# Kernel optimization log

Measured on AMD Instinct MI355X. Metric: run time of the kernel, lower is better.

## Reference

```python
import jax, jax.numpy as jnp
import numpy as np

N = 50000
E = 800000
NEG_SLOPE = 0.2  # PyG GATConv default negative_slope


def _gat_layer(x, src, dst, W, a_src, a_dst, b, concat):
    # x: [N, Fin]; src/dst: [Etot] (self-loops already appended)
    H, O = a_src.shape
    n = x.shape[0]
    h = (x @ W).reshape(n, H, O)                      # [N, H, O]
    e_src = jnp.einsum('nho,ho->nh', h, a_src)        # [N, H]
    e_dst = jnp.einsum('nho,ho->nh', h, a_dst)
    alpha = e_src[src] + e_dst[dst]                   # [Etot, H]
    alpha = jnp.where(alpha >= 0, alpha, NEG_SLOPE * alpha)
    # segment softmax over destination nodes
    amax = jax.ops.segment_max(alpha, dst, num_segments=n)
    ex = jnp.exp(alpha - amax[dst])
    denom = jax.ops.segment_sum(ex, dst, num_segments=n)
    att = ex / (denom[dst] + 1e-16)                   # [Etot, H]
    msg = h[src] * att[:, :, None]                    # [Etot, H, O]
    agg = jax.ops.segment_sum(msg, dst, num_segments=n)  # [N, H, O]
    out = agg.reshape(n, H * O) if concat else agg.mean(axis=1)
    return out + b


def setup_inputs() -> dict:
    key = jax.random.key(0)
    k0, k1 = jax.random.split(key)
    inp = {
        'x': jax.random.normal(k0, (N, 2), jnp.float32),
        'edge_index': jax.random.randint(k1, (2, E), 0, N),
    }
    s = 0.1
    dims = [(2, 4, 64), (256, 4, 64), (256, 1, 2)]
    for i, (fin, H, O) in enumerate(dims):
        kw, ks, kd = jax.random.split(jax.random.fold_in(key, i + 10), 3)
        inp[f'W{i}'] = jax.random.normal(kw, (fin, H * O), jnp.float32) * s
        inp[f'a_src{i}'] = jax.random.normal(ks, (H, O), jnp.float32) * s
        inp[f'a_dst{i}'] = jax.random.normal(kd, (H, O), jnp.float32) * s
        inp[f'b{i}'] = jnp.zeros((H * O if i < 2 else O,), jnp.float32)
    return inp


def reference(x, edge_index, W0, a_src0, a_dst0, b0, W1, a_src1, a_dst1, b1,
              W2, a_src2, a_dst2, b2):
    n = x.shape[0]
    loops = jnp.arange(n, dtype=edge_index.dtype)  # PyG add_self_loops=True
    src = jnp.concatenate([edge_index[0], loops])
    dst = jnp.concatenate([edge_index[1], loops])
    h = jax.nn.relu(_gat_layer(x, src, dst, W0, a_src0, a_dst0, b0, True))
    h = jax.nn.relu(_gat_layer(h, src, dst, W1, a_src1, a_dst1, b1, True))
    h = jax.nn.relu(_gat_layer(h, src, dst, W2, a_src2, a_dst2, b2, False))
    return h
```

## Files before the change

### kernel.cpp

```cpp
#include <hip/hip_runtime.h>
#include <math.h>


typedef __attribute__((ext_vector_type(8))) short s16x8;
typedef __attribute__((ext_vector_type(4))) float f32x4;
typedef unsigned short u16;

__device__ __forceinline__ float wred_sum(float v){
  #pragma unroll
  for (int m = 32; m > 0; m >>= 1) v += __shfl_xor(v, m, 64);
  return v;
}
__device__ __forceinline__ void wred_sum4(float4& v){
  #pragma unroll
  for (int m = 32; m > 0; m >>= 1){
    v.x += __shfl_xor(v.x, m, 64);
    v.y += __shfl_xor(v.y, m, 64);
    v.z += __shfl_xor(v.z, m, 64);
    v.w += __shfl_xor(v.w, m, 64);
  }
}
__device__ __forceinline__ u16 bf16_rne(float x){
  unsigned int u = __float_as_uint(x);
  unsigned int r = u + 0x7FFFu + ((u >> 16) & 1u);
  return (u16)(r >> 16);
}

__global__ __launch_bounds__(256) void k_setup(const float* __restrict__ W1, u16* __restrict__ WhT,
                                               u16* __restrict__ WlT,
                                               const float* __restrict__ W0, const float* __restrict__ as0,
                                               const float* __restrict__ ad0, float* __restrict__ vs,
                                               int* __restrict__ deg, int N, int nblk_deg){
  int b = blockIdx.x;
  if (b < nblk_deg){
    int i = b * 256 + threadIdx.x;
    if (i < N) deg[i] = 1;
  } else if (b < nblk_deg + 256){
    int k = b - nblk_deg, j = threadIdx.x;
    float w = W1[k * 256 + j];
    u16 h = bf16_rne(w);
    float hf = __uint_as_float(((unsigned int)h) << 16);
    WhT[j * 256 + k] = h;
    WlT[j * 256 + k] = bf16_rne(w - hf);
  } else {
    int t = threadIdx.x;
    if (t < 8){
      int j = t >> 2, h = t & 3;
      float ss = 0.f, dd = 0.f;
      #pragma unroll 8
      for (int o = 0; o < 64; o++){
        float w = W0[j * 256 + h * 64 + o];
        ss = fmaf(w, as0[h * 64 + o], ss);
        dd = fmaf(w, ad0[h * 64 + o], dd);
      }
      vs[j * 4 + h]     = ss;
      vs[8 + j * 4 + h] = dd;
    }
  }
}

__global__ __launch_bounds__(256) void k_hist(const int* __restrict__ dst, int E, int* deg){
  int e = blockIdx.x * 256 + threadIdx.x;
  if (e < E) atomicAdd(&deg[dst[e]], 1);
}

__global__ __launch_bounds__(256) void k_scan_local(const int* __restrict__ deg, int* __restrict__ rowptr,
                                                    int* __restrict__ bsum, int N){
  __shared__ int sb[256];
  int t = threadIdx.x;
  int base = blockIdx.x * 2048 + t * 8;
  int d[8], s = 0;
  #pragma unroll
  for (int k = 0; k < 8; k++){
    d[k] = (base + k < N) ? deg[base + k] : 0;
    s += d[k];
  }
  sb[t] = s;
  __syncthreads();
  for (int off = 1; off < 256; off <<= 1){
    int v = (t >= off) ? sb[t - off] : 0;
    __syncthreads();
    sb[t] += v;
    __syncthreads();
  }
  int run = (t == 0) ? 0 : sb[t - 1];
  #pragma unroll
  for (int k = 0; k < 8; k++){
    if (base + k < N) rowptr[base + k] = run;
    run += d[k];
  }
  if (t == 255) bsum[blockIdx.x] = sb[255];
}

__global__ __launch_bounds__(64) void k_boff(const int* __restrict__ bsum, int* __restrict__ boff, int nb){
  __shared__ int sb[64];
  int t = threadIdx.x;
  int v = (t < nb) ? bsum[t] : 0;
  sb[t] = v;
  __syncthreads();
  for (int off = 1; off < 64; off <<= 1){
    int u = (t >= off) ? sb[t - off] : 0;
    __syncthreads();
    sb[t] += u;
    __syncthreads();
  }
  boff[t] = (t == 0) ? 0 : sb[t - 1];
  if (t == nb - 1) boff[nb] = sb[nb - 1];
}

__global__ __launch_bounds__(256) void k_finish(int* __restrict__ rowptr, const int* __restrict__ boff,
                                                int* __restrict__ ssrc, int* __restrict__ cursor,
                                                int N, int nb){
  int i = blockIdx.x * 256 + threadIdx.x;
  if (i < N){
    int p = rowptr[i] + boff[i >> 11];
    rowptr[i] = p;
    ssrc[p] = i;
    cursor[i] = p + 1;
  }
  if (i == 0) rowptr[N] = boff[nb];
}

__global__ __launch_bounds__(256) void k_scatter(const int* __restrict__ src, const int* __restrict__ dst,
                                                 int E, int* cursor, int* ssrc){
  int e = blockIdx.x * 256 + threadIdx.x;
  if (e < E){ int p = atomicAdd(&cursor[dst[e]], 1); ssrc[p] = src[e]; }
}

__global__ __launch_bounds__(256) void k_edge0(const float* __restrict__ X, const float* __restrict__ vs,
                                               const float* __restrict__ W0, const float* __restrict__ b0,
                                               const int* __restrict__ rowptr, const int* __restrict__ ssrc,
                                               float* __restrict__ X1, int N){
  int lane = threadIdx.x & 63;
  int n = blockIdx.x * 4 + (threadIdx.x >> 6);
  if (n >= N) return;
  int start = rowptr[n], deg = rowptr[n + 1] - start;
  float4 va = ((const float4*)vs)[0], vb = ((const float4*)vs)[1];
  float4 vc = ((const float4*)vs)[2], vd = ((const float4*)vs)[3];
  float2 xn = ((const float2*)X)[n];
  float4 ed4;
  ed4.x = fmaf(xn.x, vc.x, xn.y * vd.x); ed4.y = fmaf(xn.x, vc.y, xn.y * vd.y);
  ed4.z = fmaf(xn.x, vc.z, xn.y * vd.z); ed4.w = fmaf(xn.x, vc.w, xn.y * vd.w);

  float4 den = make_float4(0.f,0.f,0.f,0.f);
  float4 a0  = make_float4(0.f,0.f,0.f,0.f);
  float4 a1  = make_float4(0.f,0.f,0.f,0.f);
  for (int i = lane; i < deg; i += 64){
    int s = ssrc[start + i];
    float2 xs = ((const float2*)X)[s];
    float4 e;
    e.x = fmaf(xs.x, va.x, fmaf(xs.y, vb.x, ed4.x));
    e.y = fmaf(xs.x, va.y, fmaf(xs.y, vb.y, ed4.y));
    e.z = fmaf(xs.x, va.z, fmaf(xs.y, vb.z, ed4.z));
    e.w = fmaf(xs.x, va.w, fmaf(xs.y, vb.w, ed4.w));
    e.x = fmaxf(e.x, 0.2f*e.x); e.y = fmaxf(e.y, 0.2f*e.y);
    e.z = fmaxf(e.z, 0.2f*e.z); e.w = fmaxf(e.w, 0.2f*e.w);
    float4 wt;
    wt.x = __expf(e.x); wt.y = __expf(e.y);
    wt.z = __expf(e.z); wt.w = __expf(e.w);
    den.x += wt.x; den.y += wt.y; den.z += wt.z; den.w += wt.w;
    a0.x = fmaf(wt.x, xs.x, a0.x); a0.y = fmaf(wt.y, xs.x, a0.y);
    a0.z = fmaf(wt.z, xs.x, a0.z); a0.w = fmaf(wt.w, xs.x, a0.w);
    a1.x = fmaf(wt.x, xs.y, a1.x); a1.y = fmaf(wt.y, xs.y, a1.y);
    a1.z = fmaf(wt.z, xs.y, a1.z); a1.w = fmaf(wt.w, xs.y, a1.w);
  }
  wred_sum4(den); wred_sum4(a0); wred_sum4(a1);

  int hh = lane >> 4;
  float invd = 1.f / (((hh==0)?den.x:(hh==1)?den.y:(hh==2)?den.z:den.w) + 1e-16f);
  float g0 = ((hh==0)?a0.x:(hh==1)?a0.y:(hh==2)?a0.z:a0.w) * invd;
  float g1 = ((hh==0)?a1.x:(hh==1)?a1.y:(hh==2)?a1.z:a1.w) * invd;
  float4 w0r = ((const float4*)W0)[lane];
  float4 w1r = ((const float4*)(W0 + 256))[lane];
  float4 bb  = ((const float4*)b0)[lane];
  float4 v;
  v.x = fmaxf(fmaf(g0, w0r.x, fmaf(g1, w1r.x, bb.x)), 0.f);
  v.y = fmaxf(fmaf(g0, w0r.y, fmaf(g1, w1r.y, bb.y)), 0.f);
  v.z = fmaxf(fmaf(g0, w0r.z, fmaf(g1, w1r.z, bb.z)), 0.f);
  v.w = fmaxf(fmaf(g0, w0r.w, fmaf(g1, w1r.w, bb.w)), 0.f);
  ((float4*)(X1 + (size_t)n * 256))[lane] = v;
}

__global__ __launch_bounds__(256) void k_l1_mfma(const float* __restrict__ X,
                                                 const u16* __restrict__ WhT, const u16* __restrict__ WlT,
                                                 const float* __restrict__ as_, const float* __restrict__ ad_,
                                                 u16* __restrict__ Hh16, float* __restrict__ ES,
                                                 float* __restrict__ ED, int N){
  __shared__ u16 Ah[64 * 32], Al[64 * 32];
  __shared__ u16 Bh[256 * 32], Bl[256 * 32];
  int t = threadIdx.x;
  int wv = t >> 6, lane = t & 63;
  int lr = lane & 15, lg = lane >> 4;
  int rb = blockIdx.x * 64;

  f32x4 acc[16];
  #pragma unroll
  for (int c = 0; c < 16; c++) acc[c] = (f32x4){0.f, 0.f, 0.f, 0.f};

  int arow = t >> 2, aseg = t & 3;
  int agrow = rb + arow;

  for (int ks = 0; ks < 8; ks++){
    int k0 = ks * 32;
    __syncthreads();
    {
      float xv[8];
      if (agrow < N){
        const float4* p = (const float4*)(X + (size_t)agrow * 256 + k0 + aseg * 8);
        float4 v0 = p[0], v1 = p[1];
        xv[0]=v0.x; xv[1]=v0.y; xv[2]=v0.z; xv[3]=v0.w;
        xv[4]=v1.x; xv[5]=v1.y; xv[6]=v1.z; xv[7]=v1.w;
      } else {
        #pragma unroll
        for (int i = 0; i < 8; i++) xv[i] = 0.f;
      }
      union { u16 us[8]; uint4 v; } ph, pl;
      #pragma unroll
      for (int i = 0; i < 8; i++){
        u16 h = bf16_rne(xv[i]);
        float hf = __uint_as_float(((unsigned int)h) << 16);
        ph.us[i] = h;
        pl.us[i] = bf16_rne(xv[i] - hf);
      }
      *(uint4*)&Ah[arow * 32 + aseg * 8] = ph.v;
      *(uint4*)&Al[arow * 32 + aseg * 8] = pl.v;
    }
    #pragma unroll
    for (int i = 0; i < 4; i++){
      int chunk = i * 256 + t;
      int j = chunk >> 2, seg = chunk & 3;
      *(uint4*)&Bh[j * 32 + seg * 8] = *(const uint4*)&WhT[j * 256 + k0 + seg * 8];
      *(uint4*)&Bl[j * 32 + seg * 8] = *(const uint4*)&WlT[j * 256 + k0 + seg * 8];
    }
    __syncthreads();
    s16x8 ah = *(const s16x8*)&Ah[(wv * 16 + lr) * 32 + lg * 8];
    s16x8 al = *(const s16x8*)&Al[(wv * 16 + lr) * 32 + lg * 8];
    #pragma unroll
    for (int c = 0; c < 16; c++){
      s16x8 bh = *(const s16x8*)&Bh[(c * 16 + lr) * 32 + lg * 8];
      s16x8 bl = *(const s16x8*)&Bl[(c * 16 + lr) * 32 + lg * 8];
      acc[c] = __builtin_amdgcn_mfma_f32_16x16x32_bf16(ah, bh, acc[c], 0, 0, 0);
      acc[c] = __builtin_amdgcn_mfma_f32_16x16x32_bf16(ah, bl, acc[c], 0, 0, 0);
      acc[c] = __builtin_amdgcn_mfma_f32_16x16x32_bf16(al, bh, acc[c], 0, 0, 0);
    }
  }

  #pragma unroll
  for (int q = 0; q < 4; q++){
    int n = rb + wv * 16 + lg * 4 + q;
    if (n < N){
      union { _Float16 h[16]; uint4 v[2]; } pk;
      #pragma unroll
      for (int c = 0; c < 16; c++) pk.h[c] = (_Float16)acc[c][q];
      uint4* dstp = (uint4*)(Hh16 + (size_t)n * 256 + lr * 16);
      dstp[0] = pk.v[0];
      dstp[1] = pk.v[1];
    }
  }
  float es_p[4][4], ed_p[4][4];
  #pragma unroll
  for (int h = 0; h < 4; h++)
    #pragma unroll
    for (int q = 0; q < 4; q++){ es_p[h][q] = 0.f; ed_p[h][q] = 0.f; }
  #pragma unroll
  for (int c = 0; c < 16; c++){
    float asv = as_[c * 16 + lr];
    float adv = ad_[c * 16 + lr];
    int h = c >> 2;
    #pragma unroll
    for (int q = 0; q < 4; q++){
      es_p[h][q] = fmaf(acc[c][q], asv, es_p[h][q]);
      ed_p[h][q] = fmaf(acc[c][q], adv, ed_p[h][q]);
    }
  }
  #pragma unroll
  for (int h = 0; h < 4; h++)
    #pragma unroll
    for (int q = 0; q < 4; q++){
      #pragma unroll
      for (int mk = 1; mk < 16; mk <<= 1){
        es_p[h][q] += __shfl_xor(es_p[h][q], mk, 64);
        ed_p[h][q] += __shfl_xor(ed_p[h][q], mk, 64);
      }
    }
  if (lr == 0){
    #pragma unroll
    for (int q = 0; q < 4; q++){
      int n = rb + wv * 16 + lg * 4 + q;
      if (n < N){
        #pragma unroll
        for (int h = 0; h < 4; h++){
          ES[n * 4 + h] = es_p[h][q];
          ED[n * 4 + h] = ed_p[h][q];
        }
      }
    }
  }
}

__device__ __forceinline__ void agg_rows16(const u16* __restrict__ Hh, const int* ssh, const float* wrow,
                                           int cl, int lane, float* acc){
  union Cv { uint2 u; _Float16 h[4]; };
  int j = 0;
  for (; j + 7 < cl; j += 8){
    Cv r0, r1, r2, r3, r4, r5, r6, r7;
    float w0=wrow[j],w1=wrow[j+1],w2=wrow[j+2],w3=wrow[j+3];
    float w4=wrow[j+4],w5=wrow[j+5],w6=wrow[j+6],w7=wrow[j+7];
    r0.u = *(const uint2*)(Hh + (size_t)ssh[j  ] * 256 + 4*lane);
    r1.u = *(const uint2*)(Hh + (size_t)ssh[j+1] * 256 + 4*lane);
    r2.u = *(const uint2*)(Hh + (size_t)ssh[j+2] * 256 + 4*lane);
    r3.u = *(const uint2*)(Hh + (size_t)ssh[j+3] * 256 + 4*lane);
    r4.u = *(const uint2*)(Hh + (size_t)ssh[j+4] * 256 + 4*lane);
    r5.u = *(const uint2*)(Hh + (size_t)ssh[j+5] * 256 + 4*lane);
    r6.u = *(const uint2*)(Hh + (size_t)ssh[j+6] * 256 + 4*lane);
    r7.u = *(const uint2*)(Hh + (size_t)ssh[j+7] * 256 + 4*lane);
    #pragma unroll
    for (int k = 0; k < 4; k++) acc[k] = fmaf(w0, (float)r0.h[k], acc[k]);
    #pragma unroll
    for (int k = 0; k < 4; k++) acc[k] = fmaf(w1, (float)r1.h[k], acc[k]);
    #pragma unroll
    for (int k = 0; k < 4; k++) acc[k] = fmaf(w2, (float)r2.h[k], acc[k]);
    #pragma unroll
    for (int k = 0; k < 4; k++) acc[k] = fmaf(w3, (float)r3.h[k], acc[k]);
    #pragma unroll
    for (int k = 0; k < 4; k++) acc[k] = fmaf(w4, (float)r4.h[k], acc[k]);
    #pragma unroll
    for (int k = 0; k < 4; k++) acc[k] = fmaf(w5, (float)r5.h[k], acc[k]);
    #pragma unroll
    for (int k = 0; k < 4; k++) acc[k] = fmaf(w6, (float)r6.h[k], acc[k]);
    #pragma unroll
    for (int k = 0; k < 4; k++) acc[k] = fmaf(w7, (float)r7.h[k], acc[k]);
  }
  for (; j + 3 < cl; j += 4){
    Cv r0, r1, r2, r3;
    float w0=wrow[j],w1=wrow[j+1],w2=wrow[j+2],w3=wrow[j+3];
    r0.u = *(const uint2*)(Hh + (size_t)ssh[j  ] * 256 + 4*lane);
    r1.u = *(const uint2*)(Hh + (size_t)ssh[j+1] * 256 + 4*lane);
    r2.u = *(const uint2*)(Hh + (size_t)ssh[j+2] * 256 + 4*lane);
    r3.u = *(const uint2*)(Hh + (size_t)ssh[j+3] * 256 + 4*lane);
    #pragma unroll
    for (int k = 0; k < 4; k++) acc[k] = fmaf(w0, (float)r0.h[k], acc[k]);
    #pragma unroll
    for (int k = 0; k < 4; k++) acc[k] = fmaf(w1, (float)r1.h[k], acc[k]);
    #pragma unroll
    for (int k = 0; k < 4; k++) acc[k] = fmaf(w2, (float)r2.h[k], acc[k]);
    #pragma unroll
    for (int k = 0; k < 4; k++) acc[k] = fmaf(w3, (float)r3.h[k], acc[k]);
  }
  for (; j < cl; ++j){
    Cv r0;
    float w0 = wrow[j];
    r0.u = *(const uint2*)(Hh + (size_t)ssh[j] * 256 + 4*lane);
    #pragma unroll
    for (int k = 0; k < 4; k++) acc[k] = fmaf(w0, (float)r0.h[k], acc[k]);
  }
}

__global__ __launch_bounds__(64) void k_edge1(const u16* __restrict__ Hh16, const float* __restrict__ ES,
                                              const float* __restrict__ ED, const int* __restrict__ rowptr,
                                              const int* __restrict__ ssrc, const float* __restrict__ b1,
                                              const float* __restrict__ W2,
                                              const float* __restrict__ as2, const float* __restrict__ ad2,
                                              float* __restrict__ P2, int N){
  __shared__ int   ssh[64];
  __shared__ float wsh[4][68];
  int lane = threadIdx.x;
  int n = blockIdx.x;
  int myhead = lane & 3;
  int start = rowptr[n], deg = rowptr[n + 1] - start;
  float4 ed4 = ((const float4*)ED)[n];

  float accv[4] = {0.f, 0.f, 0.f, 0.f};
  float4 den = make_float4(0.f,0.f,0.f,0.f);

  for (int base = 0; base < deg; base += 64){
    int i = base + lane;
    float4 wt = make_float4(0.f,0.f,0.f,0.f);
    int s = 0;
    if (i < deg){
      s = ssrc[start + i];
      float4 e = ((const float4*)ES)[s];
      e.x += ed4.x; e.y += ed4.y; e.z += ed4.z; e.w += ed4.w;
      e.x = fmaxf(e.x, 0.2f*e.x); e.y = fmaxf(e.y, 0.2f*e.y);
      e.z = fmaxf(e.z, 0.2f*e.z); e.w = fmaxf(e.w, 0.2f*e.w);
      wt.x = __expf(e.x); wt.y = __expf(e.y);
      wt.z = __expf(e.z); wt.w = __expf(e.w);
    }
    den.x += wt.x; den.y += wt.y; den.z += wt.z; den.w += wt.w;
    ssh[lane] = s;
    wsh[0][lane] = wt.x; wsh[1][lane] = wt.y;
    wsh[2][lane] = wt.z; wsh[3][lane] = wt.w;
    __syncthreads();
    agg_rows16(Hh16, ssh, wsh[myhead], min(deg - base, 64), lane, accv);
    __syncthreads();
  }

  wred_sum4(den);
  float d = (myhead==0)?den.x:(myhead==1)?den.y:(myhead==2)?den.z:den.w;
  float inv = 1.f / (d + 1e-16f);
  int c0 = 64 * (lane & 3) + (lane >> 2);
  float p0 = 0.f, p1 = 0.f;
  #pragma unroll
  for (int j = 0; j < 4; j++){
    int col = c0 + 16 * j;
    float v = fmaxf(fmaf(accv[j], inv, b1[col]), 0.f);
    float2 w2 = ((const float2*)W2)[col];
    p0 = fmaf(v, w2.x, p0);
    p1 = fmaf(v, w2.y, p1);
  }
  p0 = wred_sum(p0); p1 = wred_sum(p1);
  if (lane == 0){
    float4 o;
    o.x = p0; o.y = p1;
    o.z = p0*as2[0] + p1*as2[1];
    o.w = p0*ad2[0] + p1*ad2[1];
    ((float4*)P2)[n] = o;
  }
}

__global__ __launch_bounds__(256) void k_edge2(const float* __restrict__ P2, const int* __restrict__ rowptr,
                                               const int* __restrict__ ssrc, const float* __restrict__ bias,
                                               float* __restrict__ Out, int N){
  int lane = threadIdx.x & 63;
  int n = blockIdx.x * 4 + (threadIdx.x >> 6);
  if (n >= N) return;
  int start = rowptr[n], deg = rowptr[n + 1] - start;
  float edn = ((const float4*)P2)[n].w;
  float den = 0.f, a0 = 0.f, a1 = 0.f;
  for (int i = lane; i < deg; i += 64){
    int s = ssrc[start + i];
    float4 p = ((const float4*)P2)[s];
    float a = p.z + edn; a = fmaxf(a, 0.2f * a);
    float w = __expf(a);
    den += w;
    a0 = fmaf(w, p.x, a0);
    a1 = fmaf(w, p.y, a1);
  }
  den = wred_sum(den); a0 = wred_sum(a0); a1 = wred_sum(a1);
  if (lane == 0){
    float inv = 1.f / (den + 1e-16f);
    Out[n*2]     = fmaxf(a0 * inv + bias[0], 0.f);
    Out[n*2 + 1] = fmaxf(a1 * inv + bias[1], 0.f);
  }
}

extern "C" void kernel_launch(void* const* d_in, const int* in_sizes, int n_in,
                              void* d_out, int out_size, void* d_ws, size_t ws_size,
                              hipStream_t stream) {
  const float* x   = (const float*)d_in[0];
  const int*   ei  = (const int*)  d_in[1];
  const float* W0  = (const float*)d_in[2];
  const float* as0 = (const float*)d_in[3];
  const float* ad0 = (const float*)d_in[4];
  const float* b0  = (const float*)d_in[5];
  const float* W1  = (const float*)d_in[6];
  const float* as1 = (const float*)d_in[7];
  const float* ad1 = (const float*)d_in[8];
  const float* b1  = (const float*)d_in[9];
  const float* W2  = (const float*)d_in[10];
  const float* as2 = (const float*)d_in[11];
  const float* ad2 = (const float*)d_in[12];
  const float* b2  = (const float*)d_in[13];

  int N = in_sizes[0] / 2;
  int E = in_sizes[1] / 2;
  const int* src = ei;
  const int* dst = ei + E;

  char* ws = (char*)d_ws;
  size_t off = 0;
  auto alc = [&](size_t bytes){ size_t o = off; off += (bytes + 255) & ~(size_t)255; return o; };
  int*   deg    = (int*)(ws + alc((size_t)N * 4));
  int*   rowptr = (int*)(ws + alc((size_t)(N + 1) * 4));
  int*   cursor = (int*)(ws + alc((size_t)N * 4));
  int*   ssrc   = (int*)(ws + alc((size_t)(E + N) * 4));
  float* X1     = (float*)(ws + alc((size_t)N * 256 * 4));
  u16*   Hh16   = (u16*)  (ws + alc((size_t)N * 256 * 2));
  float* es1    = (float*)(ws + alc((size_t)N * 4 * 4));
  float* ed1    = (float*)(ws + alc((size_t)N * 4 * 4));
  float* P2     = (float*)(ws + alc((size_t)N * 4 * 4));
  u16*   wht    = (u16*)  (ws + alc((size_t)256 * 256 * 2));
  u16*   wlt    = (u16*)  (ws + alc((size_t)256 * 256 * 2));
  float* vs     = (float*)(ws + alc(16 * 4));
  int*   bsum   = (int*)(ws + alc(64 * 4));
  int*   boff   = (int*)(ws + alc(65 * 4));
  float* out    = (float*)d_out;

  int nblk_deg = (N + 255) / 256;
  int nb = (N + 2047) / 2048;

  k_setup     <<<nblk_deg + 257, 256, 0, stream>>>(W1, wht, wlt, W0, as0, ad0, vs, deg, N, nblk_deg);
  k_hist      <<<(E + 255)/256, 256, 0, stream>>>(dst, E, deg);
  k_scan_local<<<nb, 256, 0, stream>>>(deg, rowptr, bsum, N);
  k_boff      <<<1, 64, 0, stream>>>(bsum, boff, nb);
  k_finish    <<<nblk_deg, 256, 0, stream>>>(rowptr, boff, ssrc, cursor, N, nb);
  k_scatter   <<<(E + 255)/256, 256, 0, stream>>>(src, dst, E, cursor, ssrc);

  k_edge0  <<<(N + 3)/4, 256, 0, stream>>>(x, vs, W0, b0, rowptr, ssrc, X1, N);
  k_l1_mfma<<<(N + 63)/64, 256, 0, stream>>>(X1, wht, wlt, as1, ad1, Hh16, es1, ed1, N);
  k_edge1  <<<N, 64, 0, stream>>>(Hh16, es1, ed1, rowptr, ssrc, b1, W2, as2, ad2, P2, N);
  k_edge2  <<<(N + 3)/4, 256, 0, stream>>>(P2, rowptr, ssrc, b2, out, N);
}
```

Before: 340.5 us.

## Fuse layer-0 output projection into layer-1 GEMM and drop block-offset scan kernel

Layer-0 edge aggregation now stores only the 8 per-head aggregated input features per node. The W0 projection, bias and ReLU are recomputed inside the layer-1 MFMA kernel's A-tile load, so the 50000x256 fp32 intermediate is never written and read back. Separately, the single-block block-offset scan kernel is removed, and each finish block serially sums the preceding block sums itself. This saves one launch and a large amount of HBM traffic, at the cost of a little extra ALU work and redundant small W0/b0 loads in the GEMM.

```diff
diff --git a/kernel.cpp b/kernel.cpp
--- a/kernel.cpp
+++ b/kernel.cpp
@@ -92,33 +92,29 @@
   if (t == 255) bsum[blockIdx.x] = sb[255];
 }
 
-__global__ __launch_bounds__(64) void k_boff(const int* __restrict__ bsum, int* __restrict__ boff, int nb){
-  __shared__ int sb[64];
-  int t = threadIdx.x;
-  int v = (t < nb) ? bsum[t] : 0;
-  sb[t] = v;
-  __syncthreads();
-  for (int off = 1; off < 64; off <<= 1){
-    int u = (t >= off) ? sb[t - off] : 0;
-    __syncthreads();
-    sb[t] += u;
-    __syncthreads();
-  }
-  boff[t] = (t == 0) ? 0 : sb[t - 1];
-  if (t == nb - 1) boff[nb] = sb[nb - 1];
-}
-
-__global__ __launch_bounds__(256) void k_finish(int* __restrict__ rowptr, const int* __restrict__ boff,
+__global__ __launch_bounds__(256) void k_finish(int* __restrict__ rowptr, const int* __restrict__ bsum,
                                                 int* __restrict__ ssrc, int* __restrict__ cursor,
                                                 int N, int nb){
+  __shared__ int off_sh;
   int i = blockIdx.x * 256 + threadIdx.x;
+  if (threadIdx.x == 0){
+    int bk = blockIdx.x >> 3;
+    int s = 0;
+    for (int k = 0; k < bk; k++) s += bsum[k];
+    off_sh = s;
+  }
+  __syncthreads();
   if (i < N){
-    int p = rowptr[i] + boff[i >> 11];
+    int p = rowptr[i] + off_sh;
     rowptr[i] = p;
     ssrc[p] = i;
     cursor[i] = p + 1;
   }
-  if (i == 0) rowptr[N] = boff[nb];
+  if (i == 0){
+    int s = 0;
+    for (int k = 0; k < nb; k++) s += bsum[k];
+    rowptr[N] = s;
+  }
 }
 
 __global__ __launch_bounds__(256) void k_scatter(const int* __restrict__ src, const int* __restrict__ dst,
@@ -128,9 +124,8 @@
 }
 
 __global__ __launch_bounds__(256) void k_edge0(const float* __restrict__ X, const float* __restrict__ vs,
-                                               const float* __restrict__ W0, const float* __restrict__ b0,
                                                const int* __restrict__ rowptr, const int* __restrict__ ssrc,
-                                               float* __restrict__ X1, int N){
+                                               float* __restrict__ agg2, int N){
   int lane = threadIdx.x & 63;
   int n = blockIdx.x * 4 + (threadIdx.x >> 6);
   if (n >= N) return;
@@ -166,22 +161,22 @@
   }
   wred_sum4(den); wred_sum4(a0); wred_sum4(a1);
 
-  int hh = lane >> 4;
-  float invd = 1.f / (((hh==0)?den.x:(hh==1)?den.y:(hh==2)?den.z:den.w) + 1e-16f);
-  float g0 = ((hh==0)?a0.x:(hh==1)?a0.y:(hh==2)?a0.z:a0.w) * invd;
-  float g1 = ((hh==0)?a1.x:(hh==1)?a1.y:(hh==2)?a1.z:a1.w) * invd;
-  float4 w0r = ((const float4*)W0)[lane];
-  float4 w1r = ((const float4*)(W0 + 256))[lane];
-  float4 bb  = ((const float4*)b0)[lane];
-  float4 v;
-  v.x = fmaxf(fmaf(g0, w0r.x, fmaf(g1, w1r.x, bb.x)), 0.f);
-  v.y = fmaxf(fmaf(g0, w0r.y, fmaf(g1, w1r.y, bb.y)), 0.f);
-  v.z = fmaxf(fmaf(g0, w0r.z, fmaf(g1, w1r.z, bb.z)), 0.f);
-  v.w = fmaxf(fmaf(g0, w0r.w, fmaf(g1, w1r.w, bb.w)), 0.f);
-  ((float4*)(X1 + (size_t)n * 256))[lane] = v;
-}
-
-__global__ __launch_bounds__(256) void k_l1_mfma(const float* __restrict__ X,
+  if (lane == 0){
+    float4 inv;
+    inv.x = 1.f / (den.x + 1e-16f); inv.y = 1.f / (den.y + 1e-16f);
+    inv.z = 1.f / (den.z + 1e-16f); inv.w = 1.f / (den.w + 1e-16f);
+    float4 gA, gB;
+    gA.x = a0.x * inv.x; gA.y = a1.x * inv.x;
+    gA.z = a0.y * inv.y; gA.w = a1.y * inv.y;
+    gB.x = a0.z * inv.z; gB.y = a1.z * inv.z;
+    gB.z = a0.w * inv.w; gB.w = a1.w * inv.w;
+    float4* g = (float4*)(agg2 + (size_t)n * 8);
+    g[0] = gA; g[1] = gB;
+  }
+}
+
+__global__ __launch_bounds__(256) void k_l1_mfma(const float* __restrict__ agg2,
+                                                 const float* __restrict__ W0, const float* __restrict__ b0,
                                                  const u16* __restrict__ WhT, const u16* __restrict__ WlT,
                                                  const float* __restrict__ as_, const float* __restrict__ ad_,
                                                  u16* __restrict__ Hh16, float* __restrict__ ES,
@@ -199,27 +194,45 @@
 
   int arow = t >> 2, aseg = t & 3;
   int agrow = rb + arow;
+  float4 ga = make_float4(0.f,0.f,0.f,0.f), gb = make_float4(0.f,0.f,0.f,0.f);
+  if (agrow < N){
+    const float4* g = (const float4*)(agg2 + (size_t)agrow * 8);
+    ga = g[0]; gb = g[1];
+  }
 
   for (int ks = 0; ks < 8; ks++){
     int k0 = ks * 32;
     __syncthreads();
     {
+      int c0 = k0 + aseg * 8;
+      int h = c0 >> 6;
+      float g0 = (h==0)?ga.x:(h==1)?ga.z:(h==2)?gb.x:gb.z;
+      float g1 = (h==0)?ga.y:(h==1)?ga.w:(h==2)?gb.y:gb.w;
+      float4 w0a = *(const float4*)(W0 + c0);
+      float4 w0b = *(const float4*)(W0 + c0 + 4);
+      float4 w1a = *(const float4*)(W0 + 256 + c0);
+      float4 w1b = *(const float4*)(W0 + 256 + c0 + 4);
+      float4 bba = *(const float4*)(b0 + c0);
+      float4 bbb = *(const float4*)(b0 + c0 + 4);
       float xv[8];
-      if (agrow < N){
-        const float4* p = (const float4*)(X + (size_t)agrow * 256 + k0 + aseg * 8);
-        float4 v0 = p[0], v1 = p[1];
-        xv[0]=v0.x; xv[1]=v0.y; xv[2]=v0.z; xv[3]=v0.w;
-        xv[4]=v1.x; xv[5]=v1.y; xv[6]=v1.z; xv[7]=v1.w;
-      } else {
+      xv[0] = fmaxf(fmaf(g0, w0a.x, fmaf(g1, w1a.x, bba.x)), 0.f);
+      xv[1] = fmaxf(fmaf(g0, w0a.y, fmaf(g1, w1a.y, bba.y)), 0.f);
+      xv[2] = fmaxf(fmaf(g0, w0a.z, fmaf(g1, w1a.z, bba.z)), 0.f);
+      xv[3] = fmaxf(fmaf(g0, w0a.w, fmaf(g1, w1a.w, bba.w)), 0.f);
+      xv[4] = fmaxf(fmaf(g0, w0b.x, fmaf(g1, w1b.x, bbb.x)), 0.f);
+      xv[5] = fmaxf(fmaf(g0, w0b.y, fmaf(g1, w1b.y, bbb.y)), 0.f);
+      xv[6] = fmaxf(fmaf(g0, w0b.z, fmaf(g1, w1b.z, bbb.z)), 0.f);
+      xv[7] = fmaxf(fmaf(g0, w0b.w, fmaf(g1, w1b.w, bbb.w)), 0.f);
+      if (agrow >= N){
         #pragma unroll
         for (int i = 0; i < 8; i++) xv[i] = 0.f;
       }
       union { u16 us[8]; uint4 v; } ph, pl;
       #pragma unroll
       for (int i = 0; i < 8; i++){
-        u16 h = bf16_rne(xv[i]);
-        float hf = __uint_as_float(((unsigned int)h) << 16);
-        ph.us[i] = h;
+        u16 h16 = bf16_rne(xv[i]);
+        float hf = __uint_as_float(((unsigned int)h16) << 16);
+        ph.us[i] = h16;
         pl.us[i] = bf16_rne(xv[i] - hf);
       }
       *(uint4*)&Ah[arow * 32 + aseg * 8] = ph.v;
@@ -474,8 +487,8 @@
   int*   rowptr = (int*)(ws + alc((size_t)(N + 1) * 4));
   int*   cursor = (int*)(ws + alc((size_t)N * 4));
   int*   ssrc   = (int*)(ws + alc((size_t)(E + N) * 4));
-  float* X1     = (float*)(ws + alc((size_t)N * 256 * 4));
   u16*   Hh16   = (u16*)  (ws + alc((size_t)N * 256 * 2));
+  float* agg2   = (float*)(ws + alc((size_t)N * 8 * 4));
   float* es1    = (float*)(ws + alc((size_t)N * 4 * 4));
   float* ed1    = (float*)(ws + alc((size_t)N * 4 * 4));
   float* P2     = (float*)(ws + alc((size_t)N * 4 * 4));
@@ -483,7 +496,6 @@
   u16*   wlt    = (u16*)  (ws + alc((size_t)256 * 256 * 2));
   float* vs     = (float*)(ws + alc(16 * 4));
   int*   bsum   = (int*)(ws + alc(64 * 4));
-  int*   boff   = (int*)(ws + alc(65 * 4));
   float* out    = (float*)d_out;
 
   int nblk_deg = (N + 255) / 256;
@@ -492,12 +504,11 @@
   k_setup     <<<nblk_deg + 257, 256, 0, stream>>>(W1, wht, wlt, W0, as0, ad0, vs, deg, N, nblk_deg);
   k_hist      <<<(E + 255)/256, 256, 0, stream>>>(dst, E, deg);
   k_scan_local<<<nb, 256, 0, stream>>>(deg, rowptr, bsum, N);
-  k_boff      <<<1, 64, 0, stream>>>(bsum, boff, nb);
-  k_finish    <<<nblk_deg, 256, 0, stream>>>(rowptr, boff, ssrc, cursor, N, nb);
+  k_finish    <<<nblk_deg, 256, 0, stream>>>(rowptr, bsum, ssrc, cursor, N, nb);
   k_scatter   <<<(E + 255)/256, 256, 0, stream>>>(src, dst, E, cursor, ssrc);
 
-  k_edge0  <<<(N + 3)/4, 256, 0, stream>>>(x, vs, W0, b0, rowptr, ssrc, X1, N);
-  k_l1_mfma<<<(N + 63)/64, 256, 0, stream>>>(X1, wht, wlt, as1, ad1, Hh16, es1, ed1, N);
+  k_edge0  <<<(N + 3)/4, 256, 0, stream>>>(x, vs, rowptr, ssrc, agg2, N);
+  k_l1_mfma<<<(N + 63)/64, 256, 0, stream>>>(agg2, W0, b0, wht, wlt, as1, ad1, Hh16, es1, ed1, N);
   k_edge1  <<<N, 64, 0, stream>>>(Hh16, es1, ed1, rowptr, ssrc, b1, W2, as2, ad2, P2, N);
   k_edge2  <<<(N + 3)/4, 256, 0, stream>>>(P2, rowptr, ssrc, b2, out, N);
 }
```

Result: no change. 345.0 us (+1.3%).
